# Kernel tuning notes

Hardware: AMD Instinct MI355X
Metric: run time of the kernel (lower is better)

Reference implementation:

```python
import jax, jax.numpy as jnp
import numpy as np

N, C, T = 64, 512, 64
P = N * (N - 1) // 2  # 2016 pairs


def _maxpool2x2(h):
    p, c, H, W = h.shape
    return h.reshape(p, c, H // 2, 2, W // 2, 2).max(axis=(3, 5))


def setup_inputs() -> dict:
    key = jax.random.key(0)
    ks = jax.random.split(key, 16)
    s = lambda k, shape, fan: jax.random.normal(k, shape, jnp.float32) * (1.0 / np.sqrt(fan))
    return {
        "x": jax.random.normal(ks[0], (N, C, T), jnp.float32),
        "w_conv1d": s(ks[1], (256, 512), 512),  # Conv1d(512,256,k=1) weight squeezed
        "b_conv1d": jnp.zeros((256,), jnp.float32),
        "w_c1": s(ks[2], (32, 512), 512),       # Conv2d(512,32,1x1)
        "b_c1": jnp.zeros((32,), jnp.float32),
        "w_c2": s(ks[3], (8, 32), 32),          # Conv2d(32,8,1x1)
        "b_c2": jnp.zeros((8,), jnp.float32),
        "w_fc1": s(ks[4], (32, 64), 64),
        "b_fc1": jnp.zeros((32,), jnp.float32),
        "w_fc2": s(ks[5], (8, 32), 32),
        "b_fc2": jnp.zeros((8,), jnp.float32),
        "w_fc3": s(ks[6], (1, 8), 8),
        "b_fc3": jnp.zeros((1,), jnp.float32),
        "w_mlp": s(ks[7], (1, C * T), C * T),   # stand-in my_fc: Linear(512*T,1)
        "b_mlp": jnp.zeros((1,), jnp.float32),
    }


def reference(x, w_conv1d, b_conv1d, w_c1, b_c1, w_c2, b_c2,
              w_fc1, b_fc1, w_fc2, b_fc2, w_fc3, b_fc3, w_mlp, b_mlp):
    # per-sample score head (my_fc stand-in)
    score = jax.nn.sigmoid(x.reshape(N, -1) @ w_mlp.T + b_mlp)  # [N,1]
    # shared conv1d over all samples at once (original does it per-pair)
    f = jnp.einsum("nct,oc->not", x, w_conv1d) + b_conv1d[None, :, None]  # [N,256,T]
    ii, jj = jnp.triu_indices(N, k=1)  # P pairs, same order as the nested loop
    # pairwise correlation matrix: einsum('abd,acd->abc')
    M = jnp.einsum("pct,pdt->pcd", f[ii], f[jj])  # [P,256,256]
    M = M.reshape(P, 512, 32, 4)
    h = jnp.einsum("pchw,oc->pohw", M, w_c1) + b_c1[None, :, None, None]
    h = _maxpool2x2(h)  # [P,32,16,2]
    h = jnp.einsum("pchw,oc->pohw", h, w_c2) + b_c2[None, :, None, None]
    h = _maxpool2x2(h)  # [P,8,8,1]
    v = h.reshape(P, 64)
    v = jax.nn.relu(v @ w_fc1.T + b_fc1)
    v = jax.nn.relu(v @ w_fc2.T + b_fc2)
    group_score = jax.nn.sigmoid(v @ w_fc3.T + b_fc3).reshape(-1)  # [P]
    return score, group_score
```

## Files before the change

kernel.cpp:

```cpp
#include <hip/hip_runtime.h>
#include <hip/hip_bf16.h>
#include <math.h>


typedef __attribute__((ext_vector_type(8))) short short8;
typedef __attribute__((ext_vector_type(4))) float f32x4;

__device__ __forceinline__ unsigned short f2bf(float f) {
    __hip_bfloat16 h = __float2bfloat16(f);
    return *reinterpret_cast<unsigned short*>(&h);
}

__global__ __launch_bounds__(256) void k_prep(
    const float* __restrict__ x, const float* __restrict__ w_conv1d,
    const float* __restrict__ b_conv1d, const float* __restrict__ w_c1,
    unsigned short* __restrict__ xxTf, unsigned short* __restrict__ Wbf,
    float* __restrict__ Gb)
{
    __shared__ float sf[64 * 65];
    int u = blockIdx.x, tid = threadIdx.x;

    if (u < 128) {
        int idx = u * 256 + tid;
        int m = idx >> 7, c4 = (idx & 127) * 4;
        float4 v = *reinterpret_cast<const float4*>(w_conv1d + m * 512 + c4);
        ushort4 uu;
        uu.x = f2bf(v.x); uu.y = f2bf(v.y); uu.z = f2bf(v.z); uu.w = f2bf(v.w);
        int mt = m >> 4, r15 = m & 15;
        int kc = c4 >> 5, k8 = (c4 >> 3) & 3, rem = c4 & 7;
        *reinterpret_cast<ushort4*>(
            Wbf + ((mt * 16 + kc) * 64 + k8 * 16 + r15) * 8 + rem) = uu;
    } else if (u < 256) {
        int b = u - 128;
        int r = b >> 1;
        int cin = (b & 1) * 256 + tid;
        int s = r >> 5, o = r & 31;
        const float* wrow = w_c1 + o * 512 + s;
        const float* wcp  = w_conv1d + cin;
        float pq[4];
        #pragma unroll
        for (int q = 0; q < 4; ++q) {
            float acc = 0.f;
            #pragma unroll 8
            for (int c = q * 64; c < q * 64 + 64; ++c)
                acc += wrow[2 * c] * wcp[c * 512];
            pq[q] = acc;
        }
        float v = ((pq[0] + pq[1]) + pq[2]) + pq[3];
        int m = 256 + r;
        int mt = m >> 4, r15 = m & 15;
        int kc = cin >> 5, k8 = (cin >> 3) & 3, rem = cin & 7;
        Wbf[((mt * 16 + kc) * 64 + k8 * 16 + r15) * 8 + rem] = f2bf(v);
    } else if (u == 256) {
        float* abred = sf;
        Gb[tid] = b_conv1d[tid];
        int r = tid & 63, q = tid >> 6;
        int s = r >> 5, o = r & 31;
        const float* wr2 = w_c1 + o * 512 + s;
        float a = 0.f;
        #pragma unroll 8
        for (int c = q * 64; c < q * 64 + 64; ++c)
            a += wr2[2 * c] * b_conv1d[c];
        abred[tid] = a;
        __syncthreads();
        if (tid < 64)
            Gb[256 + tid] = abred[tid] + abred[tid + 64]
                          + abred[tid + 128] + abred[tid + 192];
    } else {
        int v = u - 257;
        int n = v >> 3, c0 = (v & 7) * 64;
        float* tile = sf;
        int cl = tid >> 4, t4 = (tid & 15) * 4;
        const float* xp = x + n * 32768 + c0 * 64;
        #pragma unroll
        for (int pp = 0; pp < 4; ++pp) {
            int c = cl + pp * 16;
            float4 vv = *reinterpret_cast<const float4*>(xp + c * 64 + t4);
            tile[(t4 + 0) * 65 + c] = vv.x; tile[(t4 + 1) * 65 + c] = vv.y;
            tile[(t4 + 2) * 65 + c] = vv.z; tile[(t4 + 3) * 65 + c] = vv.w;
        }
        __syncthreads();
        int tl = tid >> 4, cl4 = (tid & 15) * 4;
        int c = c0 + cl4;
        int kc = c >> 5, k8 = (c >> 3) & 3, rem = c & 7;
        #pragma unroll
        for (int pp = 0; pp < 4; ++pp) {
            int t = tl + pp * 16;
            ushort4 uu;
            uu.x = f2bf(tile[t * 65 + cl4 + 0]);
            uu.y = f2bf(tile[t * 65 + cl4 + 1]);
            uu.z = f2bf(tile[t * 65 + cl4 + 2]);
            uu.w = f2bf(tile[t * 65 + cl4 + 3]);
            *reinterpret_cast<ushort4*>(
                xxTf + n * 32768 + ((pp * 16 + kc) * 64 + k8 * 16 + tl) * 8 + rem) = uu;
        }
    }
}

__global__ __launch_bounds__(256) void k_fgemm(
    const unsigned short* __restrict__ Wbf, const unsigned short* __restrict__ xxTf,
    const float* __restrict__ Gb, unsigned short* __restrict__ FTTb,
    unsigned short* __restrict__ ALb)
{
    int n = blockIdx.x, mg = blockIdx.y, nt = blockIdx.z;
    int tid = threadIdx.x, l = tid & 63, w = tid >> 6;
    int mt = mg * 4 + w;
    int m0 = mt * 16;
    int t0 = nt * 16;
    int r15 = l & 15, kg = l >> 4;
    const unsigned short* ap = Wbf + (size_t)mt * 16 * 512 + l * 8;
    const unsigned short* bp = xxTf + (size_t)n * 32768 + (size_t)nt * 16 * 512 + l * 8;
    f32x4 acc = {0.f, 0.f, 0.f, 0.f};
    #pragma unroll
    for (int ks = 0; ks < 16; ++ks) {
        short8 a = *reinterpret_cast<const short8*>(ap + ks * 512);
        short8 b = *reinterpret_cast<const short8*>(bp + ks * 512);
        acc = __builtin_amdgcn_mfma_f32_16x16x32_bf16(a, b, acc, 0, 0, 0);
    }
    int t = t0 + r15;
    int mrow = m0 + kg * 4;
    float4 gb = *reinterpret_cast<const float4*>(Gb + mrow);
    float gbv[4] = {gb.x, gb.y, gb.z, gb.w};
    if (m0 < 256) {
        #pragma unroll
        for (int r = 0; r < 4; ++r) {
            int m = mrow + r;
            int e = m & 127, s = m >> 7, kp = s * 64 + t;
            int off = (((e << 8) + (kp << 1)) ^ ((e & 7) << 4)) >> 1;
            FTTb[n * 16384 + off] = f2bf(acc[r] + gbv[r]);
        }
    } else {
        #pragma unroll
        for (int r = 0; r < 4; ++r) {
            int m = mrow + r;
            int rr = m - 256, o = rr & 31, sA = rr >> 5, kp = sA * 64 + t;
            int off = (((o << 8) + (kp << 1)) ^ ((o & 7) << 4)) >> 1;
            ALb[n * 4096 + off] = f2bf(acc[r] + gbv[r]);
        }
    }
}

__global__ __launch_bounds__(256) void k_pairs(
    const char* __restrict__ FTTb, const char* __restrict__ ALb,
    const float* __restrict__ b_c1, const float* __restrict__ w_c2,
    const float* __restrict__ b_c2, const float* __restrict__ w_fc1,
    const float* __restrict__ b_fc1, const float* __restrict__ w_fc2,
    const float* __restrict__ b_fc2, const float* __restrict__ w_fc3,
    const float* __restrict__ b_fc3, const float* __restrict__ x,
    const float* __restrict__ w_mlp, const float* __restrict__ bm,
    float* __restrict__ out)
{
    __shared__ uint4 smq[2560];
    char* sm = (char*)smq;
    int tid = threadIdx.x;

    if (blockIdx.x < 64) {
        int n = blockIdx.x;
        float* red   = (float*)sm;
        float* parts = (float*)sm + 4;
        const float4* xb = reinterpret_cast<const float4*>(x + n * 32768);
        const float4* wb = reinterpret_cast<const float4*>(w_mlp);
        #pragma unroll
        for (int c4 = 0; c4 < 4; ++c4) {
            const float4* x4 = xb + c4 * 2048;
            const float4* w4 = wb + c4 * 2048;
            float acc = 0.f;
            for (int u = tid; u < 2048; u += 256) {
                float4 a = x4[u], w = w4[u];
                acc += a.x * w.x + a.y * w.y + a.z * w.z + a.w * w.w;
            }
            for (int off = 32; off; off >>= 1) acc += __shfl_down(acc, off, 64);
            if ((tid & 63) == 0) red[tid >> 6] = acc;
            __syncthreads();
            if (tid == 0) parts[c4] = red[0] + red[1] + red[2] + red[3];
            __syncthreads();
        }
        if (tid == 0) {
            float s = parts[0] + parts[1] + parts[2] + parts[3] + bm[0];
            out[n] = 1.f / (1.f + expf(-s));
        }
        return;
    }

    int p = blockIdx.x - 64;
    int i = 0, rem = p;
    while (rem >= 63 - i) { rem -= 63 - i; ++i; }
    int j = i + 1 + rem;

    {
        const uint4* sA = reinterpret_cast<const uint4*>(ALb + (size_t)i * 8192);
        uint4* dA = reinterpret_cast<uint4*>(sm);
        #pragma unroll
        for (int u = 0; u < 2; ++u) dA[tid + 256 * u] = sA[tid + 256 * u];
        const uint4* sB = reinterpret_cast<const uint4*>(FTTb + (size_t)j * 32768);
        uint4* dB = reinterpret_cast<uint4*>(sm + 8192);
        #pragma unroll
        for (int u = 0; u < 8; ++u) dB[tid + 256 * u] = sB[tid + 256 * u];
    }
    __syncthreads();

    int l = tid & 63, wid = tid >> 6;
    int col = l & 15;
    int lk16 = (l >> 4) << 4;
    int xr = (col & 7) << 4;
    int oa0 = col, oa1 = col + 16;
    int e0 = wid * 32 + col, e1 = e0 + 16;

    f32x4 acc00 = {0.f,0.f,0.f,0.f}, acc01 = {0.f,0.f,0.f,0.f};
    f32x4 acc10 = {0.f,0.f,0.f,0.f}, acc11 = {0.f,0.f,0.f,0.f};
    #pragma unroll
    for (int ks = 0; ks < 4; ++ks) {
        int kb = ks * 64 + lk16;
        short8 a0 = *reinterpret_cast<const short8*>(sm + (((oa0 << 8) + kb) ^ xr));
        short8 a1 = *reinterpret_cast<const short8*>(sm + (((oa1 << 8) + kb) ^ xr));
        short8 b0 = *reinterpret_cast<const short8*>(sm + 8192 + (((e0 << 8) + kb) ^ xr));
        short8 b1 = *reinterpret_cast<const short8*>(sm + 8192 + (((e1 << 8) + kb) ^ xr));
        acc00 = __builtin_amdgcn_mfma_f32_16x16x32_bf16(a0, b0, acc00, 0, 0, 0);
        acc01 = __builtin_amdgcn_mfma_f32_16x16x32_bf16(a0, b1, acc01, 0, 0, 0);
        acc10 = __builtin_amdgcn_mfma_f32_16x16x32_bf16(a1, b0, acc10, 0, 0, 0);
        acc11 = __builtin_amdgcn_mfma_f32_16x16x32_bf16(a1, b1, acc11, 0, 0, 0);
    }
    __syncthreads();

    float* H = (float*)sm;
    int rowbase = (l >> 4) * 4;
    #pragma unroll
    for (int r4 = 0; r4 < 4; ++r4) {
        int o0 = rowbase + r4, o1 = o0 + 16;
        float bb0 = b_c1[o0], bb1 = b_c1[o1];
        H[o0 * 132 + e0] = acc00[r4] + bb0;
        H[o0 * 132 + e1] = acc01[r4] + bb0;
        H[o1 * 132 + e0] = acc10[r4] + bb1;
        H[o1 * 132 + e1] = acc11[r4] + bb1;
    }
    __syncthreads();

    float* PL = (float*)(sm + 17408);
    for (int idx = tid; idx < 1024; idx += 256) {
        int o = idx >> 5, h2 = (idx >> 1) & 15, w2 = idx & 1;
        const float* hp = H + o * 132 + h2 * 8 + w2 * 2;
        PL[o * 32 + h2 * 2 + w2] =
            fmaxf(fmaxf(hp[0], hp[1]), fmaxf(hp[4], hp[5]));
    }
    __syncthreads();

    float* C2 = (float*)(sm + 21504);
    {
        int o2 = tid >> 5, pos = tid & 31;
        float a2 = b_c2[o2];
        #pragma unroll 8
        for (int o = 0; o < 32; ++o) a2 += w_c2[o2 * 32 + o] * PL[o * 32 + pos];
        C2[o2 * 32 + pos] = a2;
    }
    __syncthreads();

    float* V = (float*)(sm + 22528);
    if (tid < 64) {
        int o2 = tid >> 3, h3 = tid & 7;
        const float* cp = C2 + o2 * 32 + h3 * 4;
        V[tid] = fmaxf(fmaxf(cp[0], cp[1]), fmaxf(cp[2], cp[3]));
    }
    __syncthreads();

    float* R1 = (float*)(sm + 22784);
    if (tid < 32) {
        float a = b_fc1[tid];
        const float* wr = w_fc1 + tid * 64;
        #pragma unroll 8
        for (int u = 0; u < 64; ++u) a += wr[u] * V[u];
        R1[tid] = fmaxf(a, 0.f);
    }
    __syncthreads();

    float* R2 = (float*)(sm + 22912);
    if (tid < 8) {
        float a = b_fc2[tid];
        #pragma unroll 8
        for (int u = 0; u < 32; ++u) a += w_fc2[tid * 32 + u] * R1[u];
        R2[tid] = fmaxf(a, 0.f);
    }
    __syncthreads();

    if (tid == 0) {
        float a = b_fc3[0];
        #pragma unroll
        for (int u = 0; u < 8; ++u) a += w_fc3[u] * R2[u];
        out[64 + p] = 1.f / (1.f + expf(-a));
    }
}

extern "C" void kernel_launch(void* const* d_in, const int* in_sizes, int n_in,
                              void* d_out, int out_size, void* d_ws, size_t ws_size,
                              hipStream_t stream) {
    const float* x        = (const float*)d_in[0];
    const float* w_conv1d = (const float*)d_in[1];
    const float* b_conv1d = (const float*)d_in[2];
    const float* w_c1     = (const float*)d_in[3];
    const float* b_c1     = (const float*)d_in[4];
    const float* w_c2     = (const float*)d_in[5];
    const float* b_c2     = (const float*)d_in[6];
    const float* w_fc1    = (const float*)d_in[7];
    const float* b_fc1    = (const float*)d_in[8];
    const float* w_fc2    = (const float*)d_in[9];
    const float* b_fc2    = (const float*)d_in[10];
    const float* w_fc3    = (const float*)d_in[11];
    const float* b_fc3    = (const float*)d_in[12];
    const float* w_mlp    = (const float*)d_in[13];
    const float* b_mlp    = (const float*)d_in[14];
    float* out = (float*)d_out;

    char* base = (char*)d_ws;
    unsigned short* xxTf = (unsigned short*)(base);
    unsigned short* FTTb = (unsigned short*)(base + 4194304);
    unsigned short* ALb  = (unsigned short*)(base + 6291456);
    unsigned short* Wbf  = (unsigned short*)(base + 6815744);
    float*          Gb   = (float*)(base + 7143424);

    hipLaunchKernelGGL(k_prep, dim3(769), dim3(256), 0, stream,
                       x, w_conv1d, b_conv1d, w_c1, xxTf, Wbf, Gb);
    hipLaunchKernelGGL(k_fgemm, dim3(64, 5, 4), dim3(256), 0, stream,
                       Wbf, xxTf, Gb, FTTb, ALb);
    hipLaunchKernelGGL(k_pairs, dim3(2080), dim3(256), 0, stream,
                       (const char*)FTTb, (const char*)ALb,
                       b_c1, w_c2, b_c2, w_fc1, b_fc1,
                       w_fc2, b_fc2, w_fc3, b_fc3, x, w_mlp, b_mlp, out);
}
```

Baseline: 124.7 us.

## Fuse x transpose/bf16 conversion into fgemm and move score head there

Drops the separate transpose-and-convert pass over x in k_prep and its intermediate bf16 workspace buffer. k_fgemm now loads and converts its x tile into shared memory directly, and each block computes all five M-groups so the tile is reused. The per-sample sigmoid score head moves from k_pairs into k_fgemm, so k_pairs only handles the pair blocks. This removes one global round trip over x, at the cost of fewer, heavier fgemm blocks (320) and 5 accumulators per wave.

New measurement: 131.0 us. +5.0%, slower.

```diff
diff --git a/kernel.cpp b/kernel.cpp
--- a/kernel.cpp
+++ b/kernel.cpp
@@ -12,12 +12,11 @@
 }
 
 __global__ __launch_bounds__(256) void k_prep(
-    const float* __restrict__ x, const float* __restrict__ w_conv1d,
-    const float* __restrict__ b_conv1d, const float* __restrict__ w_c1,
-    unsigned short* __restrict__ xxTf, unsigned short* __restrict__ Wbf,
-    float* __restrict__ Gb)
+    const float* __restrict__ w_conv1d, const float* __restrict__ b_conv1d,
+    const float* __restrict__ w_c1,
+    unsigned short* __restrict__ Wbf, float* __restrict__ Gb)
 {
-    __shared__ float sf[64 * 65];
+    __shared__ float abred[256];
     int u = blockIdx.x, tid = threadIdx.x;
 
     if (u < 128) {
@@ -51,8 +50,7 @@
         int mt = m >> 4, r15 = m & 15;
         int kc = cin >> 5, k8 = (cin >> 3) & 3, rem = cin & 7;
         Wbf[((mt * 16 + kc) * 64 + k8 * 16 + r15) * 8 + rem] = f2bf(v);
-    } else if (u == 256) {
-        float* abred = sf;
+    } else {
         Gb[tid] = b_conv1d[tid];
         int r = tid & 63, q = tid >> 6;
         int s = r >> 5, o = r & 31;
@@ -66,98 +64,22 @@
         if (tid < 64)
             Gb[256 + tid] = abred[tid] + abred[tid + 64]
                           + abred[tid + 128] + abred[tid + 192];
-    } else {
-        int v = u - 257;
-        int n = v >> 3, c0 = (v & 7) * 64;
-        float* tile = sf;
-        int cl = tid >> 4, t4 = (tid & 15) * 4;
-        const float* xp = x + n * 32768 + c0 * 64;
-        #pragma unroll
-        for (int pp = 0; pp < 4; ++pp) {
-            int c = cl + pp * 16;
-            float4 vv = *reinterpret_cast<const float4*>(xp + c * 64 + t4);
-            tile[(t4 + 0) * 65 + c] = vv.x; tile[(t4 + 1) * 65 + c] = vv.y;
-            tile[(t4 + 2) * 65 + c] = vv.z; tile[(t4 + 3) * 65 + c] = vv.w;
-        }
-        __syncthreads();
-        int tl = tid >> 4, cl4 = (tid & 15) * 4;
-        int c = c0 + cl4;
-        int kc = c >> 5, k8 = (c >> 3) & 3, rem = c & 7;
-        #pragma unroll
-        for (int pp = 0; pp < 4; ++pp) {
-            int t = tl + pp * 16;
-            ushort4 uu;
-            uu.x = f2bf(tile[t * 65 + cl4 + 0]);
-            uu.y = f2bf(tile[t * 65 + cl4 + 1]);
-            uu.z = f2bf(tile[t * 65 + cl4 + 2]);
-            uu.w = f2bf(tile[t * 65 + cl4 + 3]);
-            *reinterpret_cast<ushort4*>(
-                xxTf + n * 32768 + ((pp * 16 + kc) * 64 + k8 * 16 + tl) * 8 + rem) = uu;
-        }
     }
 }
 
 __global__ __launch_bounds__(256) void k_fgemm(
-    const unsigned short* __restrict__ Wbf, const unsigned short* __restrict__ xxTf,
+    const unsigned short* __restrict__ Wbf, const float* __restrict__ x,
     const float* __restrict__ Gb, unsigned short* __restrict__ FTTb,
-    unsigned short* __restrict__ ALb)
+    unsigned short* __restrict__ ALb, const float* __restrict__ w_mlp,
+    const float* __restrict__ bm, float* __restrict__ out)
 {
-    int n = blockIdx.x, mg = blockIdx.y, nt = blockIdx.z;
-    int tid = threadIdx.x, l = tid & 63, w = tid >> 6;
-    int mt = mg * 4 + w;
-    int m0 = mt * 16;
-    int t0 = nt * 16;
-    int r15 = l & 15, kg = l >> 4;
-    const unsigned short* ap = Wbf + (size_t)mt * 16 * 512 + l * 8;
-    const unsigned short* bp = xxTf + (size_t)n * 32768 + (size_t)nt * 16 * 512 + l * 8;
-    f32x4 acc = {0.f, 0.f, 0.f, 0.f};
-    #pragma unroll
-    for (int ks = 0; ks < 16; ++ks) {
-        short8 a = *reinterpret_cast<const short8*>(ap + ks * 512);
-        short8 b = *reinterpret_cast<const short8*>(bp + ks * 512);
-        acc = __builtin_amdgcn_mfma_f32_16x16x32_bf16(a, b, acc, 0, 0, 0);
-    }
-    int t = t0 + r15;
-    int mrow = m0 + kg * 4;
-    float4 gb = *reinterpret_cast<const float4*>(Gb + mrow);
-    float gbv[4] = {gb.x, gb.y, gb.z, gb.w};
-    if (m0 < 256) {
-        #pragma unroll
-        for (int r = 0; r < 4; ++r) {
-            int m = mrow + r;
-            int e = m & 127, s = m >> 7, kp = s * 64 + t;
-            int off = (((e << 8) + (kp << 1)) ^ ((e & 7) << 4)) >> 1;
-            FTTb[n * 16384 + off] = f2bf(acc[r] + gbv[r]);
-        }
-    } else {
-        #pragma unroll
-        for (int r = 0; r < 4; ++r) {
-            int m = mrow + r;
-            int rr = m - 256, o = rr & 31, sA = rr >> 5, kp = sA * 64 + t;
-            int off = (((o << 8) + (kp << 1)) ^ ((o & 7) << 4)) >> 1;
-            ALb[n * 4096 + off] = f2bf(acc[r] + gbv[r]);
-        }
-    }
-}
-
-__global__ __launch_bounds__(256) void k_pairs(
-    const char* __restrict__ FTTb, const char* __restrict__ ALb,
-    const float* __restrict__ b_c1, const float* __restrict__ w_c2,
-    const float* __restrict__ b_c2, const float* __restrict__ w_fc1,
-    const float* __restrict__ b_fc1, const float* __restrict__ w_fc2,
-    const float* __restrict__ b_fc2, const float* __restrict__ w_fc3,
-    const float* __restrict__ b_fc3, const float* __restrict__ x,
-    const float* __restrict__ w_mlp, const float* __restrict__ bm,
-    float* __restrict__ out)
-{
-    __shared__ uint4 smq[2560];
-    char* sm = (char*)smq;
-    int tid = threadIdx.x;
-
-    if (blockIdx.x < 64) {
-        int n = blockIdx.x;
-        float* red   = (float*)sm;
-        float* parts = (float*)sm + 4;
+    __shared__ __align__(16) unsigned short xt[16 * 520];
+    int bid = blockIdx.x, tid = threadIdx.x;
+
+    if (bid >= 256) {
+        int n = bid - 256;
+        float* red   = (float*)xt;
+        float* parts = (float*)xt + 4;
         const float4* xb = reinterpret_cast<const float4*>(x + n * 32768);
         const float4* wb = reinterpret_cast<const float4*>(w_mlp);
         #pragma unroll
@@ -182,10 +104,83 @@
         return;
     }
 
-    int p = blockIdx.x - 64;
+    int n = bid >> 2, nt = bid & 3;
+    int t0 = nt * 16;
+
+    {
+        int j = tid & 3, cl = tid >> 2;
+        const float* xp = x + n * 32768 + t0 + j * 4;
+        #pragma unroll
+        for (int pass = 0; pass < 8; ++pass) {
+            int c = pass * 64 + cl;
+            float4 v = *reinterpret_cast<const float4*>(xp + c * 64);
+            xt[(4 * j + 0) * 520 + c] = f2bf(v.x);
+            xt[(4 * j + 1) * 520 + c] = f2bf(v.y);
+            xt[(4 * j + 2) * 520 + c] = f2bf(v.z);
+            xt[(4 * j + 3) * 520 + c] = f2bf(v.w);
+        }
+    }
+    __syncthreads();
+
+    int l = tid & 63, w = tid >> 6;
+    int r15 = l & 15, kg = l >> 4;
+    const unsigned short* abase = Wbf + l * 8;
+
+    f32x4 acc[5] = {};
+    #pragma unroll
+    for (int ks = 0; ks < 16; ++ks) {
+        short8 b = *reinterpret_cast<const short8*>(xt + r15 * 520 + ks * 32 + kg * 8);
+        #pragma unroll
+        for (int mg = 0; mg < 5; ++mg) {
+            int mt = mg * 4 + w;
+            short8 a = *reinterpret_cast<const short8*>(
+                abase + ((size_t)(mt * 16 + ks)) * 512);
+            acc[mg] = __builtin_amdgcn_mfma_f32_16x16x32_bf16(a, b, acc[mg], 0, 0, 0);
+        }
+    }
+
+    int t = t0 + r15;
+    #pragma unroll
+    for (int mg = 0; mg < 5; ++mg) {
+        int mt = mg * 4 + w, m0 = mt * 16;
+        int mrow = m0 + kg * 4;
+        float4 gb = *reinterpret_cast<const float4*>(Gb + mrow);
+        float gbv[4] = {gb.x, gb.y, gb.z, gb.w};
+        if (m0 < 256) {
+            #pragma unroll
+            for (int r = 0; r < 4; ++r) {
+                int m = mrow + r;
+                int e = m & 127, s = m >> 7, kp = s * 64 + t;
+                int off = (((e << 8) + (kp << 1)) ^ ((e & 7) << 4)) >> 1;
+                FTTb[n * 16384 + off] = f2bf(acc[mg][r] + gbv[r]);
+            }
+        } else {
+            #pragma unroll
+            for (int r = 0; r < 4; ++r) {
+                int m = mrow + r;
+                int rr = m - 256, o = rr & 31, sA = rr >> 5, kp = sA * 64 + t;
+                int off = (((o << 8) + (kp << 1)) ^ ((o & 7) << 4)) >> 1;
+                ALb[n * 4096 + off] = f2bf(acc[mg][r] + gbv[r]);
+            }
+        }
+    }
+}
+
+__global__ __launch_bounds__(256) void k_pairs(
+    const char* __restrict__ FTTb, const char* __restrict__ ALb,
+    const float* __restrict__ b_c1, const float* __restrict__ w_c2,
+    const float* __restrict__ b_c2, const float* __restrict__ w_fc1,
+    const float* __restrict__ b_fc1, const float* __restrict__ w_fc2,
+    const float* __restrict__ b_fc2, const float* __restrict__ w_fc3,
+    const float* __restrict__ b_fc3, float* __restrict__ out)
+{
+    __shared__ uint4 smq[2560];
+    char* sm = (char*)smq;
+    int p = blockIdx.x;
     int i = 0, rem = p;
     while (rem >= 63 - i) { rem -= 63 - i; ++i; }
     int j = i + 1 + rem;
+    int tid = threadIdx.x;
 
     {
         const uint4* sA = reinterpret_cast<const uint4*>(ALb + (size_t)i * 8192);
@@ -310,18 +305,17 @@
     float* out = (float*)d_out;
 
     char* base = (char*)d_ws;
-    unsigned short* xxTf = (unsigned short*)(base);
-    unsigned short* FTTb = (unsigned short*)(base + 4194304);
-    unsigned short* ALb  = (unsigned short*)(base + 6291456);
-    unsigned short* Wbf  = (unsigned short*)(base + 6815744);
-    float*          Gb   = (float*)(base + 7143424);
-
-    hipLaunchKernelGGL(k_prep, dim3(769), dim3(256), 0, stream,
-                       x, w_conv1d, b_conv1d, w_c1, xxTf, Wbf, Gb);
-    hipLaunchKernelGGL(k_fgemm, dim3(64, 5, 4), dim3(256), 0, stream,
-                       Wbf, xxTf, Gb, FTTb, ALb);
-    hipLaunchKernelGGL(k_pairs, dim3(2080), dim3(256), 0, stream,
+    unsigned short* FTTb = (unsigned short*)(base);
+    unsigned short* ALb  = (unsigned short*)(base + 2097152);
+    unsigned short* Wbf  = (unsigned short*)(base + 2621440);
+    float*          Gb   = (float*)(base + 2949120);
+
+    hipLaunchKernelGGL(k_prep, dim3(257), dim3(256), 0, stream,
+                       w_conv1d, b_conv1d, w_c1, Wbf, Gb);
+    hipLaunchKernelGGL(k_fgemm, dim3(320), dim3(256), 0, stream,
+                       Wbf, x, Gb, FTTb, ALb, w_mlp, b_mlp, out);
+    hipLaunchKernelGGL(k_pairs, dim3(2016), dim3(256), 0, stream,
                        (const char*)FTTb, (const char*)ALb,
                        b_c1, w_c2, b_c2, w_fc1, b_fc1,
-                       w_fc2, b_fc2, w_fc3, b_fc3, x, w_mlp, b_mlp, out);
-}
+                       w_fc2, b_fc2, w_fc3, b_fc3, out);
+}
```
